# Optimization experiments

Hardware: AMD Instinct MI355X
Metric: run time of the kernel (lower is better)

The kernel has to match this reference:

```python
import jax, jax.numpy as jnp
import numpy as np

B = 1048576  # batch size
D = 16       # in_dim == hid_dim == out_dim (required by the torch matmul broadcasting)


def setup_inputs() -> dict:
    key = jax.random.key(0)
    kx, kw = jax.random.split(key)
    x = jax.random.normal(kx, (B, D), dtype=jnp.float32)
    W = jax.random.normal(kw, (D, D, D), dtype=jnp.float32) * (1.0 / D)
    return {"x": x, "W": W}


def reference(x, W):
    # Original torch: xBx = x @ W @ x.T permuted, then take the batch diagonal.
    # Mathematically: out[b, k] = sum_{i, j} x[b, i] * W[k, i, j] * x[b, j]
    # (batched bilinear/quadratic form per output channel k). We compute only
    # the needed diagonal terms instead of the full BxB cross-batch product.
    return jnp.einsum('bi,kij,bj->bk', x, W, x)
```

## Files before the change

### kernel.cpp

```cpp
#include <hip/hip_runtime.h>
#include <hip/hip_bf16.h>


typedef __attribute__((ext_vector_type(8)))  short  short8;
typedef __attribute__((ext_vector_type(8)))  __bf16 bf16x8;
typedef __attribute__((ext_vector_type(4)))  float  floatx4;

#define DEV static __device__ __forceinline__

constexpr int pair_base(int i) { return i * 16 - (i * (i - 1)) / 2; }
constexpr int pi_of(int p) { int i = 0; while (pair_base(i + 1) <= p) ++i; return i; }
constexpr int pj_of(int p) { return pi_of(p) + (p - pair_base(pi_of(p))); }

template <int P>
DEV float pval(const float* xv) {
    if constexpr (P >= 136) {
        return 0.f;
    } else {
        constexpr int I = pi_of(P);
        constexpr int J = pj_of(P);
        return xv[I] * xv[J];
    }
}

template <int BASE>
DEV short8 make_afrag(const float* xv) {
    union { short8 s; __hip_bfloat162 h[4]; } u;
    u.h[0] = __float22bfloat162_rn(make_float2(pval<BASE + 0>(xv), pval<BASE + 1>(xv)));
    u.h[1] = __float22bfloat162_rn(make_float2(pval<BASE + 2>(xv), pval<BASE + 3>(xv)));
    u.h[2] = __float22bfloat162_rn(make_float2(pval<BASE + 4>(xv), pval<BASE + 5>(xv)));
    u.h[3] = __float22bfloat162_rn(make_float2(pval<BASE + 6>(xv), pval<BASE + 7>(xv)));
    return u.s;
}

template <int H>
DEV void build_afrags(const float* xv, short8& a0, short8& a1, short8& a2,
                      short8& a3, short8& a4) {
    a0 = make_afrag<0 * 32 + H * 8>(xv);
    a1 = make_afrag<1 * 32 + H * 8>(xv);
    a2 = make_afrag<2 * 32 + H * 8>(xv);
    a3 = make_afrag<3 * 32 + H * 8>(xv);
    a4 = make_afrag<4 * 32 + H * 8>(xv);
}

DEV floatx4 mfma_bf16(short8 a, short8 b, floatx4 c) {
    return __builtin_amdgcn_mfma_f32_16x16x32_bf16(
        __builtin_bit_cast(bf16x8, a), __builtin_bit_cast(bf16x8, b), c, 0, 0, 0);
}

__global__ __launch_bounds__(256, 4)
void bilinear16_kernel(const float* __restrict__ x, const float* __restrict__ W,
                       float* __restrict__ out, int ntiles) {
    __shared__ __align__(16) short Qt[16][160];
    const int tid = threadIdx.x;
    for (int idx = tid; idx < 16 * 160; idx += 256) {
        const int n = idx / 160;
        const int p = idx - n * 160;
        float q = 0.f;
        if (p < 136) {
            int i = 0, rem = p;
            while (rem >= 16 - i) { rem -= 16 - i; ++i; }
            const int j = i + rem;
            q = W[n * 256 + i * 16 + j];
            if (i != j) q += W[n * 256 + j * 16 + i];
        }
        __hip_bfloat16 h = __float2bfloat16(q);
        Qt[n][p] = *reinterpret_cast<short*>(&h);
    }
    __syncthreads();

    const int lane = tid & 63;
    const int n    = lane & 15;
    const int quad = lane >> 4;

    const short8 b0 = *reinterpret_cast<const short8*>(&Qt[n][0 * 32 + quad * 8]);
    const short8 b1 = *reinterpret_cast<const short8*>(&Qt[n][1 * 32 + quad * 8]);
    const short8 b2 = *reinterpret_cast<const short8*>(&Qt[n][2 * 32 + quad * 8]);
    const short8 b3 = *reinterpret_cast<const short8*>(&Qt[n][3 * 32 + quad * 8]);
    const short8 b4 = *reinterpret_cast<const short8*>(&Qt[n][4 * 32 + quad * 8]);

    const int waveId = blockIdx.x * 4 + (tid >> 6);
    const int nwaves = gridDim.x * 4;

    for (int t = waveId; t < ntiles; t += nwaves) {
        const float4* xr = reinterpret_cast<const float4*>(x + (size_t)(t * 16 + n) * 16);
        const float4 c0 = xr[0], c1 = xr[1], c2 = xr[2], c3 = xr[3];
        float xv[16] = {c0.x, c0.y, c0.z, c0.w, c1.x, c1.y, c1.z, c1.w,
                        c2.x, c2.y, c2.z, c2.w, c3.x, c3.y, c3.z, c3.w};

        short8 a0, a1, a2, a3, a4;
        if      (quad == 0) build_afrags<0>(xv, a0, a1, a2, a3, a4);
        else if (quad == 1) build_afrags<1>(xv, a0, a1, a2, a3, a4);
        else if (quad == 2) build_afrags<2>(xv, a0, a1, a2, a3, a4);
        else                build_afrags<3>(xv, a0, a1, a2, a3, a4);

        floatx4 acc = {0.f, 0.f, 0.f, 0.f};
        acc = mfma_bf16(a0, b0, acc);
        acc = mfma_bf16(a1, b1, acc);
        acc = mfma_bf16(a2, b2, acc);
        acc = mfma_bf16(a3, b3, acc);
        acc = mfma_bf16(a4, b4, acc);

        float* orow = out + (size_t)(t * 16 + quad * 4) * 16 + n;
        orow[0]  = acc[0];
        orow[16] = acc[1];
        orow[32] = acc[2];
        orow[48] = acc[3];
    }
}

extern "C" void kernel_launch(void* const* d_in, const int* in_sizes, int n_in,
                              void* d_out, int out_size, void* d_ws, size_t ws_size,
                              hipStream_t stream) {
    const float* x = (const float*)d_in[0];
    const float* W = (const float*)d_in[1];
    float* out = (float*)d_out;
    const int Bn = in_sizes[0] / 16;
    const int ntiles = Bn >> 4;
    bilinear16_kernel<<<1024, 256, 0, stream>>>(x, W, out, ntiles);
}
```

Baseline: 139.0 us.

## Use cyclic pair enumeration so each lane builds fragments without quad branching

Reorders the 136 upper-triangular products into a cyclic enumeration. Each 16-lane quad owns a rotated set of index pairs (offset 4*q), so every lane computes the same compile-time pattern of products from only three float4 loads. The pairs that are shared between quads get half weight. This removes the divergent four-way branch over quad and cuts per-lane loads from four float4 to three. The launch grid is also doubled to 2048 blocks. The packed W table is rebuilt to match, which adds index arithmetic to the one-time setup.

```diff
diff --git a/kernel.cpp b/kernel.cpp
--- a/kernel.cpp
+++ b/kernel.cpp
@@ -8,39 +8,24 @@
 
 #define DEV static __device__ __forceinline__
 
-constexpr int pair_base(int i) { return i * 16 - (i * (i - 1)) / 2; }
-constexpr int pi_of(int p) { int i = 0; while (pair_base(i + 1) <= p) ++i; return i; }
-constexpr int pj_of(int p) { return pi_of(p) + (p - pair_base(pi_of(p))); }
+constexpr int  alpha_of(int c) { return (c < 32) ? (c & 3) : (c - 32); }
+constexpr int  beta_of(int c)  { return (c < 32) ? ((c & 3) + (c >> 2)) : (c - 32 + 8); }
+constexpr bool live_of(int c)  { return c < 36; }
 
-template <int P>
+template <int C>
 DEV float pval(const float* xv) {
-    if constexpr (P >= 136) {
-        return 0.f;
-    } else {
-        constexpr int I = pi_of(P);
-        constexpr int J = pj_of(P);
-        return xv[I] * xv[J];
-    }
+    if constexpr (!live_of(C)) return 0.f;
+    else return xv[alpha_of(C)] * xv[beta_of(C)];
 }
 
-template <int BASE>
+template <int S>
 DEV short8 make_afrag(const float* xv) {
     union { short8 s; __hip_bfloat162 h[4]; } u;
-    u.h[0] = __float22bfloat162_rn(make_float2(pval<BASE + 0>(xv), pval<BASE + 1>(xv)));
-    u.h[1] = __float22bfloat162_rn(make_float2(pval<BASE + 2>(xv), pval<BASE + 3>(xv)));
-    u.h[2] = __float22bfloat162_rn(make_float2(pval<BASE + 4>(xv), pval<BASE + 5>(xv)));
-    u.h[3] = __float22bfloat162_rn(make_float2(pval<BASE + 6>(xv), pval<BASE + 7>(xv)));
+    u.h[0] = __float22bfloat162_rn(make_float2(pval<8 * S + 0>(xv), pval<8 * S + 1>(xv)));
+    u.h[1] = __float22bfloat162_rn(make_float2(pval<8 * S + 2>(xv), pval<8 * S + 3>(xv)));
+    u.h[2] = __float22bfloat162_rn(make_float2(pval<8 * S + 4>(xv), pval<8 * S + 5>(xv)));
+    u.h[3] = __float22bfloat162_rn(make_float2(pval<8 * S + 6>(xv), pval<8 * S + 7>(xv)));
     return u.s;
-}
-
-template <int H>
-DEV void build_afrags(const float* xv, short8& a0, short8& a1, short8& a2,
-                      short8& a3, short8& a4) {
-    a0 = make_afrag<0 * 32 + H * 8>(xv);
-    a1 = make_afrag<1 * 32 + H * 8>(xv);
-    a2 = make_afrag<2 * 32 + H * 8>(xv);
-    a3 = make_afrag<3 * 32 + H * 8>(xv);
-    a4 = make_afrag<4 * 32 + H * 8>(xv);
 }
 
 DEV floatx4 mfma_bf16(short8 a, short8 b, floatx4 c) {
@@ -55,44 +40,50 @@
     const int tid = threadIdx.x;
     for (int idx = tid; idx < 16 * 160; idx += 256) {
         const int n = idx / 160;
-        const int p = idx - n * 160;
-        float q = 0.f;
-        if (p < 136) {
-            int i = 0, rem = p;
-            while (rem >= 16 - i) { rem -= 16 - i; ++i; }
-            const int j = i + rem;
-            q = W[n * 256 + i * 16 + j];
-            if (i != j) q += W[n * 256 + j * 16 + i];
+        const int k = idx - n * 160;
+        const int s = k >> 5, q = (k >> 3) & 3, j = k & 7;
+        const int c = 8 * s + j;
+        float qv = 0.f;
+        if (c < 36) {
+            const int a = (c < 32) ? (c & 3) : (c - 32);
+            const int b = (c < 32) ? ((c & 3) + (c >> 2)) : (c - 32 + 8);
+            const float w = (c < 32) ? 1.0f : 0.5f;
+            const int I = (a + 4 * q) & 15, J = (b + 4 * q) & 15;
+            qv = (I == J) ? W[n * 256 + I * 16 + I]
+                          : w * (W[n * 256 + I * 16 + J] + W[n * 256 + J * 16 + I]);
         }
-        __hip_bfloat16 h = __float2bfloat16(q);
-        Qt[n][p] = *reinterpret_cast<short*>(&h);
+        __hip_bfloat16 h = __float2bfloat16(qv);
+        Qt[n][k] = *reinterpret_cast<short*>(&h);
     }
     __syncthreads();
 
     const int lane = tid & 63;
     const int n    = lane & 15;
-    const int quad = lane >> 4;
+    const int q    = lane >> 4;
 
-    const short8 b0 = *reinterpret_cast<const short8*>(&Qt[n][0 * 32 + quad * 8]);
-    const short8 b1 = *reinterpret_cast<const short8*>(&Qt[n][1 * 32 + quad * 8]);
-    const short8 b2 = *reinterpret_cast<const short8*>(&Qt[n][2 * 32 + quad * 8]);
-    const short8 b3 = *reinterpret_cast<const short8*>(&Qt[n][3 * 32 + quad * 8]);
-    const short8 b4 = *reinterpret_cast<const short8*>(&Qt[n][4 * 32 + quad * 8]);
+    const short8 b0 = *reinterpret_cast<const short8*>(&Qt[n][0 * 32 + q * 8]);
+    const short8 b1 = *reinterpret_cast<const short8*>(&Qt[n][1 * 32 + q * 8]);
+    const short8 b2 = *reinterpret_cast<const short8*>(&Qt[n][2 * 32 + q * 8]);
+    const short8 b3 = *reinterpret_cast<const short8*>(&Qt[n][3 * 32 + q * 8]);
+    const short8 b4 = *reinterpret_cast<const short8*>(&Qt[n][4 * 32 + q * 8]);
 
     const int waveId = blockIdx.x * 4 + (tid >> 6);
     const int nwaves = gridDim.x * 4;
 
     for (int t = waveId; t < ntiles; t += nwaves) {
         const float4* xr = reinterpret_cast<const float4*>(x + (size_t)(t * 16 + n) * 16);
-        const float4 c0 = xr[0], c1 = xr[1], c2 = xr[2], c3 = xr[3];
-        float xv[16] = {c0.x, c0.y, c0.z, c0.w, c1.x, c1.y, c1.z, c1.w,
-                        c2.x, c2.y, c2.z, c2.w, c3.x, c3.y, c3.z, c3.w};
+        const float4 c0 = xr[q];
+        const float4 c1 = xr[(q + 1) & 3];
+        const float4 c2 = xr[(q + 2) & 3];
+        const float xv[12] = {c0.x, c0.y, c0.z, c0.w,
+                              c1.x, c1.y, c1.z, c1.w,
+                              c2.x, c2.y, c2.z, c2.w};
 
-        short8 a0, a1, a2, a3, a4;
-        if      (quad == 0) build_afrags<0>(xv, a0, a1, a2, a3, a4);
-        else if (quad == 1) build_afrags<1>(xv, a0, a1, a2, a3, a4);
-        else if (quad == 2) build_afrags<2>(xv, a0, a1, a2, a3, a4);
-        else                build_afrags<3>(xv, a0, a1, a2, a3, a4);
+        const short8 a0 = make_afrag<0>(xv);
+        const short8 a1 = make_afrag<1>(xv);
+        const short8 a2 = make_afrag<2>(xv);
+        const short8 a3 = make_afrag<3>(xv);
+        const short8 a4 = make_afrag<4>(xv);
 
         floatx4 acc = {0.f, 0.f, 0.f, 0.f};
         acc = mfma_bf16(a0, b0, acc);
@@ -101,7 +92,7 @@
         acc = mfma_bf16(a3, b3, acc);
         acc = mfma_bf16(a4, b4, acc);
 
-        float* orow = out + (size_t)(t * 16 + quad * 4) * 16 + n;
+        float* orow = out + (size_t)(t * 16 + q * 4) * 16 + n;
         orow[0]  = acc[0];
         orow[16] = acc[1];
         orow[32] = acc[2];
@@ -117,5 +108,5 @@
     float* out = (float*)d_out;
     const int Bn = in_sizes[0] / 16;
     const int ntiles = Bn >> 4;
-    bilinear16_kernel<<<1024, 256, 0, stream>>>(x, W, out, ntiles);
+    bilinear16_kernel<<<2048, 256, 0, stream>>>(x, W, out, ntiles);
 }
```

Measured after the change: 127.2 us. -8.5%, faster.
